# Performance work log

Hardware: AMD Instinct MI355X
Metric: run time of the kernel (lower is better)

Reference implementation:

```python
import jax, jax.numpy as jnp
import numpy as np

N_NODES = 50000
N_EDGES = 800000
D_FEAT = 128
DIM_H = 128
N_LAYERS = 3
N_CLASSES = 10
N_GRAPHS = 512


def setup_inputs() -> dict:
    key = jax.random.key(0)
    ks = jax.random.split(key, 8)
    x = jax.random.normal(ks[0], (N_NODES, D_FEAT), dtype=jnp.float32)
    W = jax.random.normal(ks[1], (N_LAYERS, DIM_H, DIM_H), dtype=jnp.float32) * 0.1
    b = jnp.zeros((N_LAYERS, DIM_H), dtype=jnp.float32)
    lin_w = jax.random.normal(ks[2], (DIM_H, N_CLASSES), dtype=jnp.float32) * 0.1
    lin_b = jnp.zeros((N_CLASSES,), dtype=jnp.float32)
    edge_index = jax.random.randint(ks[3], (2, N_EDGES), 0, N_NODES, dtype=jnp.int64)
    batch = jnp.sort(jax.random.randint(ks[4], (N_NODES,), 0, N_GRAPHS, dtype=jnp.int64))
    return {"x": x, "W": W, "b": b, "lin_w": lin_w, "lin_b": lin_b,
            "edge_index": edge_index, "batch": batch, "num_layers": N_LAYERS}


def _gcn_norm(edge_index, n_nodes):
    # add self loops (PyG GCNConv default), then symmetric normalization
    loop = jnp.arange(n_nodes, dtype=edge_index.dtype)
    src = jnp.concatenate([edge_index[0], loop])  # [E+N]
    dst = jnp.concatenate([edge_index[1], loop])
    deg = jax.ops.segment_sum(jnp.ones_like(dst, dtype=jnp.float32), dst,
                              num_segments=n_nodes)
    dinv = jnp.where(deg > 0, jax.lax.rsqrt(deg), 0.0)
    norm = dinv[src] * dinv[dst]  # [E+N]
    return src, dst, norm


def _gcn_conv(h, Wi, bi, src, dst, norm, n_nodes):
    h = h @ Wi                       # [N, dim_h] dense GEMM
    msg = h[src] * norm[:, None]     # gather + scale, [E+N, dim_h]
    out = jax.ops.segment_sum(msg, dst, num_segments=n_nodes)  # scatter-add
    return out + bi


def reference(x, W, b, lin_w, lin_b, edge_index, batch, num_layers):
    n_nodes = x.shape[0]
    src, dst, norm = _gcn_norm(edge_index, n_nodes)
    h = x
    for i in range(num_layers):
        h = jax.nn.relu(_gcn_conv(h, W[i], b[i], src, dst, norm, n_nodes))
    # global mean pool over graph ids
    sums = jax.ops.segment_sum(h, batch, num_segments=N_GRAPHS)          # [G, dim_h]
    cnts = jax.ops.segment_sum(jnp.ones((n_nodes,), h.dtype), batch,
                               num_segments=N_GRAPHS)
    hG = sums / jnp.maximum(cnts, 1.0)[:, None]
    # dropout is identity at eval; num_layers > 1 branch applies the linear head
    logits = hG @ lin_w + lin_b
    return hG, jax.nn.log_softmax(logits, axis=1)
```

## Files before the change

### kernel.cpp

```cpp
#include <hip/hip_runtime.h>
#include <hip/hip_bf16.h>
#include <hip/hip_fp8.h>

#define NN 50000
#define NE 800000
#define FD 128
#define NG 512
#define NC 10
#define NL 3
#define CAP 64
#define WT_B 192
#define E1_B 3125
#define GEMM_B 782

typedef unsigned short u16;
typedef unsigned char u8;
typedef unsigned int u32;
typedef short bf16x8 __attribute__((ext_vector_type(8)));
typedef float f32x4 __attribute__((ext_vector_type(4)));

__device__ __forceinline__ float b2f(u16 v) {
    union { u32 u; float f; } c; c.u = ((u32)v) << 16; return c.f;
}
__device__ __forceinline__ u16 f2b(float f) {
    __hip_bfloat16 h = __float2bfloat16(f);
    return *(u16*)&h;
}
__device__ __forceinline__ float p2f(u8 b) {
    __hip_fp8_e4m3 h; h.__x = b; return (float)h;
}
__device__ __forceinline__ u8 f2p(float f) {
    __hip_fp8_e4m3 h(f); return h.__x;
}

__global__ __launch_bounds__(256) void k_fillcvt(const int* __restrict__ src,
                                                 const int* __restrict__ dst,
                                                 int* __restrict__ cnt,
                                                 int* __restrict__ bkt,
                                                 const float* __restrict__ W,
                                                 u16* __restrict__ wt) {
    const int bid = blockIdx.x;
    if (bid < E1_B) {
        const int e = bid * 256 + threadIdx.x;
        const int d = dst[e];
        const int slot = atomicAdd(&cnt[d], 1);
        if (slot < CAP) bkt[d * CAP + slot] = src[e];
    } else {
        const int i = (bid - E1_B) * 256 + threadIdx.x;
        const int l = i >> 14, r = i & 16383, k = r >> 7, n = r & 127;
        wt[(l << 14) + n * FD + k] = f2b(W[i]);
    }
}

__global__ __launch_bounds__(256) void k_gemm0(const float* __restrict__ x,
                                               const u16* __restrict__ WT,
                                               const int* __restrict__ cnt,
                                               float* __restrict__ dinv,
                                               u8* __restrict__ Bout) {
    const int wid = blockIdx.x * 4 + (threadIdx.x >> 6);
    if (wid >= 3125) return;
    const int row0 = wid * 16;
    const int lane = threadIdx.x & 63;
    const int m = lane & 15;
    const int q = lane >> 4;
    f32x4 acc[8];
#pragma unroll
    for (int ct = 0; ct < 8; ++ct) acc[ct] = (f32x4){0.f, 0.f, 0.f, 0.f};
    const float* arow = x + (size_t)(row0 + m) * FD + q * 8;
    const u16* wrow = WT + (size_t)m * FD + q * 8;
#pragma unroll
    for (int kb = 0; kb < 4; ++kb) {
        const float4 p0 = *(const float4*)(arow + kb * 32);
        const float4 p1 = *(const float4*)(arow + kb * 32 + 4);
        bf16x8 af;
        af[0] = (short)f2b(p0.x); af[1] = (short)f2b(p0.y);
        af[2] = (short)f2b(p0.z); af[3] = (short)f2b(p0.w);
        af[4] = (short)f2b(p1.x); af[5] = (short)f2b(p1.y);
        af[6] = (short)f2b(p1.z); af[7] = (short)f2b(p1.w);
#pragma unroll
        for (int ct = 0; ct < 8; ++ct) {
            bf16x8 bf = *(const bf16x8*)(wrow + (size_t)ct * 16 * FD + kb * 32);
            acc[ct] = __builtin_amdgcn_mfma_f32_16x16x32_bf16(af, bf, acc[ct], 0, 0, 0);
        }
    }
    float dsc[4];
#pragma unroll
    for (int r = 0; r < 4; ++r) {
        dsc[r] = rsqrtf((float)(cnt[row0 + q * 4 + r] + 1));
        if (m == 0) dinv[row0 + q * 4 + r] = dsc[r];
    }
#pragma unroll
    for (int ct = 0; ct < 8; ++ct)
#pragma unroll
        for (int r = 0; r < 4; ++r)
            Bout[(size_t)(row0 + q * 4 + r) * FD + ct * 16 + m] =
                f2p(acc[ct][r] * dsc[r]);
}

__device__ __forceinline__ float4 gather_node4(const int rs, const int re,
                                               const int* __restrict__ bkt,
                                               const u8* __restrict__ B,
                                               const float di, const int n,
                                               const float4 bb, const int f) {
    const uchar4 vs = *(const uchar4*)(B + (size_t)n * FD + f);
    float a0 = 0.f, a1 = 0.f, a2 = 0.f, a3 = 0.f;
    float b0 = 0.f, b1 = 0.f, b2 = 0.f, b3 = 0.f;
    float c0 = 0.f, c1 = 0.f, c2 = 0.f, c3 = 0.f;
    float d0 = 0.f, d1 = 0.f, d2 = 0.f, d3 = 0.f;
    int e = rs;
    for (; e + 4 <= re; e += 4) {
        const int s0 = bkt[e];
        const int s1 = bkt[e + 1];
        const int s2 = bkt[e + 2];
        const int s3 = bkt[e + 3];
        const uchar4 v0 = *(const uchar4*)(B + (size_t)s0 * FD + f);
        const uchar4 v1 = *(const uchar4*)(B + (size_t)s1 * FD + f);
        const uchar4 v2 = *(const uchar4*)(B + (size_t)s2 * FD + f);
        const uchar4 v3 = *(const uchar4*)(B + (size_t)s3 * FD + f);
        a0 += p2f(v0.x); a1 += p2f(v0.y); a2 += p2f(v0.z); a3 += p2f(v0.w);
        b0 += p2f(v1.x); b1 += p2f(v1.y); b2 += p2f(v1.z); b3 += p2f(v1.w);
        c0 += p2f(v2.x); c1 += p2f(v2.y); c2 += p2f(v2.z); c3 += p2f(v2.w);
        d0 += p2f(v3.x); d1 += p2f(v3.y); d2 += p2f(v3.z); d3 += p2f(v3.w);
    }
    for (; e < re; ++e) {
        const int s0 = bkt[e];
        const uchar4 v0 = *(const uchar4*)(B + (size_t)s0 * FD + f);
        a0 += p2f(v0.x); a1 += p2f(v0.y); a2 += p2f(v0.z); a3 += p2f(v0.w);
    }
    a0 += b0 + c0 + d0 + p2f(vs.x);
    a1 += b1 + c1 + d1 + p2f(vs.y);
    a2 += b2 + c2 + d2 + p2f(vs.z);
    a3 += b3 + c3 + d3 + p2f(vs.w);
    float4 r;
    r.x = fmaxf(a0 * di + bb.x, 0.f);
    r.y = fmaxf(a1 * di + bb.y, 0.f);
    r.z = fmaxf(a2 * di + bb.z, 0.f);
    r.w = fmaxf(a3 * di + bb.w, 0.f);
    return r;
}

__global__ __launch_bounds__(512) void k_gg(const int* __restrict__ cnt,
                                            const int* __restrict__ bkt,
                                            const u8* __restrict__ Bin,
                                            const float* __restrict__ dinv,
                                            const float* __restrict__ bias,
                                            const u16* __restrict__ WTn,
                                            u8* __restrict__ Bout) {
    __shared__ u16 sA[16][FD + 8];
    const int tid = threadIdx.x;
    const int wave = tid >> 6;
    const int lane = tid & 63;
    const int nb = blockIdx.x * 16;
    {
        const int half = lane >> 5;
        const int n = nb + wave * 2 + half;
        const int f = (lane & 31) * 4;
        const int rs = n * CAP;
        const int re = rs + cnt[n];
        const float di = dinv[n];
        const float4 bb = *(const float4*)(bias + f);
        const float4 r = gather_node4(rs, re, bkt, Bin, di, n, bb, f);
        ushort4 o;
        o.x = f2b(r.x); o.y = f2b(r.y); o.z = f2b(r.z); o.w = f2b(r.w);
        *(ushort4*)&sA[wave * 2 + half][f] = o;
    }
    __syncthreads();
    const int ct = wave;
    const int m = lane & 15;
    const int q = lane >> 4;
    f32x4 acc = (f32x4){0.f, 0.f, 0.f, 0.f};
    const u16* wrow = WTn + (size_t)m * FD + q * 8 + (size_t)ct * 16 * FD;
#pragma unroll
    for (int kb = 0; kb < 4; ++kb) {
        bf16x8 af = *(const bf16x8*)&sA[m][q * 8 + kb * 32];
        bf16x8 bf = *(const bf16x8*)(wrow + kb * 32);
        acc = __builtin_amdgcn_mfma_f32_16x16x32_bf16(af, bf, acc, 0, 0, 0);
    }
    float dsc[4];
#pragma unroll
    for (int r = 0; r < 4; ++r) dsc[r] = dinv[nb + q * 4 + r];
#pragma unroll
    for (int r = 0; r < 4; ++r)
        Bout[(size_t)(nb + q * 4 + r) * FD + ct * 16 + m] =
            f2p(acc[r] * dsc[r]);
}

__global__ __launch_bounds__(1024) void k_gpool(const int* __restrict__ cnt,
                                                const int* __restrict__ bkt,
                                                const u8* __restrict__ B,
                                                const float* __restrict__ dinv,
                                                const float* __restrict__ bias,
                                                const int* __restrict__ batch,
                                                const float* __restrict__ lin_w,
                                                const float* __restrict__ lin_b,
                                                float* __restrict__ out) {
    __shared__ float sfeat[32][FD + 4];
    __shared__ float hm[FD];
    __shared__ int bnd[2];
    __shared__ float part2[2 * NC];
    const int g = blockIdx.x;
    const int tid = threadIdx.x;
    const int lane = tid & 63;
    const int slot = (tid >> 6) * 2 + (lane >> 5);
    const int f = (lane & 31) * 4;
    if (tid < 2) {
        const int key = g + tid;
        int lo = 0, hi = NN;
        while (lo < hi) {
            const int mid = (lo + hi) >> 1;
            if (batch[mid] < key) lo = mid + 1; else hi = mid;
        }
        bnd[tid] = lo;
    }
    __syncthreads();
    const int r0 = bnd[0], r1 = bnd[1];
    const float4 bb = *(const float4*)(bias + f);
    float s0 = 0.f, s1 = 0.f, s2 = 0.f, s3 = 0.f;
    for (int r = r0 + slot; r < r1; r += 32) {
        const int rs = r * CAP;
        const float4 v = gather_node4(rs, rs + cnt[r], bkt, B,
                                      dinv[r], r, bb, f);
        s0 += v.x; s1 += v.y; s2 += v.z; s3 += v.w;
    }
    sfeat[slot][f] = s0;
    sfeat[slot][f + 1] = s1;
    sfeat[slot][f + 2] = s2;
    sfeat[slot][f + 3] = s3;
    __syncthreads();
    if (tid < 128) {
        float tot = 0.f;
#pragma unroll
        for (int s = 0; s < 32; ++s) tot += sfeat[s][tid];
        const float mean = tot / fmaxf((float)(r1 - r0), 1.0f);
        hm[tid] = mean;
        out[(size_t)g * FD + tid] = mean;
    }
    __syncthreads();
    if (tid < 128) {
        const float hv = hm[tid];
        const int wv = tid >> 6;
#pragma unroll
        for (int c = 0; c < NC; ++c) {
            float p = hv * lin_w[tid * NC + c];
#pragma unroll
            for (int o = 32; o > 0; o >>= 1) p += __shfl_down(p, o, 64);
            if ((tid & 63) == 0) part2[c * 2 + wv] = p;
        }
    }
    __syncthreads();
    if (tid == 0) {
        float lg[NC];
        float m = -1e30f;
#pragma unroll
        for (int c = 0; c < NC; ++c) {
            lg[c] = part2[2 * c] + part2[2 * c + 1] + lin_b[c];
            m = fmaxf(m, lg[c]);
        }
        float s = 0.f;
#pragma unroll
        for (int c = 0; c < NC; ++c) s += expf(lg[c] - m);
        const float lse = m + logf(s);
        float* o = out + (size_t)NG * FD + (size_t)g * NC;
#pragma unroll
        for (int c = 0; c < NC; ++c) o[c] = lg[c] - lse;
    }
}

extern "C" void kernel_launch(void* const* d_in, const int* in_sizes, int n_in,
                              void* d_out, int out_size, void* d_ws, size_t ws_size,
                              hipStream_t stream) {
    const float* x     = (const float*)d_in[0];
    const float* W     = (const float*)d_in[1];
    const float* bias  = (const float*)d_in[2];
    const float* lin_w = (const float*)d_in[3];
    const float* lin_b = (const float*)d_in[4];
    const int*   src   = (const int*)d_in[5];
    const int*   dst   = src + NE;
    const int*   batch = (const int*)d_in[6];

    u8*    B0     = (u8*)d_ws;
    u8*    B1     = B0 + (size_t)NN * FD;
    u16*   WT     = (u16*)(B1 + (size_t)NN * FD);
    int*   bkt    = (int*)(WT + (size_t)NL * FD * FD);
    int*   cnt    = bkt + (size_t)NN * CAP;
    float* dinv   = (float*)(cnt + NN);
    float* out    = (float*)d_out;

    hipMemsetAsync(cnt, 0, NN * sizeof(int), stream);
    k_fillcvt<<<E1_B + WT_B, 256, 0, stream>>>(src, dst, cnt, bkt, W, WT);
    k_gemm0<<<GEMM_B, 256, 0, stream>>>(x, WT, cnt, dinv, B0);

    k_gg<<<NN / 16, 512, 0, stream>>>(cnt, bkt, B0, dinv, bias,
                                      WT + (size_t)1 * FD * FD, B1);
    k_gg<<<NN / 16, 512, 0, stream>>>(cnt, bkt, B1, dinv, bias + FD,
                                      WT + (size_t)2 * FD * FD, B0);
    k_gpool<<<NG, 1024, 0, stream>>>(cnt, bkt, B0, dinv, bias + 2 * FD,
                                     batch, lin_w, lin_b, out);
}
```

Before: 257.3 us.

## Fuse edge bucketing and first GEMM into one kernel, apply source normalization at gather

Merges the edge-bucket fill, weight transpose, and layer-0 GEMM into a single interleaved launch. The layer-0 GEMM now reads fp32 W directly with strided loads and no longer needs degree counts. Because of that, the source-side degree scaling moves out of the GEMM epilogue and into the gather, where each neighbor's rsqrt(cnt+1) is recomputed per edge. This drops one kernel launch and the dinv array, and lets bucket atomics overlap the GEMM. In exchange it adds an extra random cnt load per edge and keeps fp8 storage of the values before normalization, which changes their scaling.

New measurement: 263.9 us. 1.03x slower.

```diff
diff --git a/kernel.cpp b/kernel.cpp
--- a/kernel.cpp
+++ b/kernel.cpp
@@ -9,9 +9,10 @@
 #define NC 10
 #define NL 3
 #define CAP 64
-#define WT_B 192
 #define E1_B 3125
 #define GEMM_B 782
+#define CVT_B 128
+#define FRONT_B 4550
 
 typedef unsigned short u16;
 typedef unsigned char u8;
@@ -33,72 +34,72 @@
     __hip_fp8_e4m3 h(f); return h.__x;
 }
 
-__global__ __launch_bounds__(256) void k_fillcvt(const int* __restrict__ src,
-                                                 const int* __restrict__ dst,
-                                                 int* __restrict__ cnt,
-                                                 int* __restrict__ bkt,
-                                                 const float* __restrict__ W,
-                                                 u16* __restrict__ wt) {
+__global__ __launch_bounds__(256) void k_front(const int* __restrict__ src,
+                                               const int* __restrict__ dst,
+                                               int* __restrict__ cnt,
+                                               int* __restrict__ bkt,
+                                               const float* __restrict__ W,
+                                               u16* __restrict__ wt,
+                                               const float* __restrict__ x,
+                                               u8* __restrict__ Bout) {
     const int bid = blockIdx.x;
-    if (bid < E1_B) {
-        const int e = bid * 256 + threadIdx.x;
+    const int r5 = bid % 5;
+    const int q5 = bid / 5;
+    if (r5 != 0) {
+        const int sid = q5 * 4 + (r5 - 1);
+        if (sid >= E1_B) return;
+        const int e = sid * 256 + threadIdx.x;
         const int d = dst[e];
         const int slot = atomicAdd(&cnt[d], 1);
         if (slot < CAP) bkt[d * CAP + slot] = src[e];
+    } else if (q5 < GEMM_B) {
+        const int wid = q5 * 4 + (threadIdx.x >> 6);
+        if (wid >= 3125) return;
+        const int row0 = wid * 16;
+        const int lane = threadIdx.x & 63;
+        const int m = lane & 15;
+        const int q = lane >> 4;
+        f32x4 acc[8];
+#pragma unroll
+        for (int ct = 0; ct < 8; ++ct) acc[ct] = (f32x4){0.f, 0.f, 0.f, 0.f};
+        const float* arow = x + (size_t)(row0 + m) * FD + q * 8;
+        const float* wbase = W + (size_t)q * 8 * FD + m;
+#pragma unroll
+        for (int kb = 0; kb < 4; ++kb) {
+            const float4 p0 = *(const float4*)(arow + kb * 32);
+            const float4 p1 = *(const float4*)(arow + kb * 32 + 4);
+            bf16x8 af;
+            af[0] = (short)f2b(p0.x); af[1] = (short)f2b(p0.y);
+            af[2] = (short)f2b(p0.z); af[3] = (short)f2b(p0.w);
+            af[4] = (short)f2b(p1.x); af[5] = (short)f2b(p1.y);
+            af[6] = (short)f2b(p1.z); af[7] = (short)f2b(p1.w);
+#pragma unroll
+            for (int ct = 0; ct < 8; ++ct) {
+                const float* wp = wbase + (size_t)kb * 32 * FD + ct * 16;
+                bf16x8 bf;
+#pragma unroll
+                for (int j = 0; j < 8; ++j)
+                    bf[j] = (short)f2b(wp[(size_t)j * FD]);
+                acc[ct] = __builtin_amdgcn_mfma_f32_16x16x32_bf16(af, bf,
+                                                                  acc[ct], 0, 0, 0);
+            }
+        }
+#pragma unroll
+        for (int ct = 0; ct < 8; ++ct)
+#pragma unroll
+            for (int r = 0; r < 4; ++r)
+                Bout[(size_t)(row0 + q * 4 + r) * FD + ct * 16 + m] =
+                    f2p(acc[ct][r]);
     } else {
-        const int i = (bid - E1_B) * 256 + threadIdx.x;
-        const int l = i >> 14, r = i & 16383, k = r >> 7, n = r & 127;
-        wt[(l << 14) + n * FD + k] = f2b(W[i]);
-    }
-}
-
-__global__ __launch_bounds__(256) void k_gemm0(const float* __restrict__ x,
-                                               const u16* __restrict__ WT,
-                                               const int* __restrict__ cnt,
-                                               float* __restrict__ dinv,
-                                               u8* __restrict__ Bout) {
-    const int wid = blockIdx.x * 4 + (threadIdx.x >> 6);
-    if (wid >= 3125) return;
-    const int row0 = wid * 16;
-    const int lane = threadIdx.x & 63;
-    const int m = lane & 15;
-    const int q = lane >> 4;
-    f32x4 acc[8];
-#pragma unroll
-    for (int ct = 0; ct < 8; ++ct) acc[ct] = (f32x4){0.f, 0.f, 0.f, 0.f};
-    const float* arow = x + (size_t)(row0 + m) * FD + q * 8;
-    const u16* wrow = WT + (size_t)m * FD + q * 8;
-#pragma unroll
-    for (int kb = 0; kb < 4; ++kb) {
-        const float4 p0 = *(const float4*)(arow + kb * 32);
-        const float4 p1 = *(const float4*)(arow + kb * 32 + 4);
-        bf16x8 af;
-        af[0] = (short)f2b(p0.x); af[1] = (short)f2b(p0.y);
-        af[2] = (short)f2b(p0.z); af[3] = (short)f2b(p0.w);
-        af[4] = (short)f2b(p1.x); af[5] = (short)f2b(p1.y);
-        af[6] = (short)f2b(p1.z); af[7] = (short)f2b(p1.w);
-#pragma unroll
-        for (int ct = 0; ct < 8; ++ct) {
-            bf16x8 bf = *(const bf16x8*)(wrow + (size_t)ct * 16 * FD + kb * 32);
-            acc[ct] = __builtin_amdgcn_mfma_f32_16x16x32_bf16(af, bf, acc[ct], 0, 0, 0);
-        }
-    }
-    float dsc[4];
-#pragma unroll
-    for (int r = 0; r < 4; ++r) {
-        dsc[r] = rsqrtf((float)(cnt[row0 + q * 4 + r] + 1));
-        if (m == 0) dinv[row0 + q * 4 + r] = dsc[r];
-    }
-#pragma unroll
-    for (int ct = 0; ct < 8; ++ct)
-#pragma unroll
-        for (int r = 0; r < 4; ++r)
-            Bout[(size_t)(row0 + q * 4 + r) * FD + ct * 16 + m] =
-                f2p(acc[ct][r] * dsc[r]);
+        const int c = (q5 - GEMM_B) * 256 + threadIdx.x + FD * FD;
+        const int l = c >> 14, rr = c & 16383, k = rr >> 7, n = rr & 127;
+        wt[(l << 14) + n * FD + k] = f2b(W[c]);
+    }
 }
 
 __device__ __forceinline__ float4 gather_node4(const int rs, const int re,
                                                const int* __restrict__ bkt,
+                                               const int* __restrict__ cnt,
                                                const u8* __restrict__ B,
                                                const float di, const int n,
                                                const float4 bb, const int f) {
@@ -113,36 +114,45 @@
         const int s1 = bkt[e + 1];
         const int s2 = bkt[e + 2];
         const int s3 = bkt[e + 3];
+        const float w0 = rsqrtf((float)(cnt[s0] + 1));
+        const float w1 = rsqrtf((float)(cnt[s1] + 1));
+        const float w2 = rsqrtf((float)(cnt[s2] + 1));
+        const float w3 = rsqrtf((float)(cnt[s3] + 1));
         const uchar4 v0 = *(const uchar4*)(B + (size_t)s0 * FD + f);
         const uchar4 v1 = *(const uchar4*)(B + (size_t)s1 * FD + f);
         const uchar4 v2 = *(const uchar4*)(B + (size_t)s2 * FD + f);
         const uchar4 v3 = *(const uchar4*)(B + (size_t)s3 * FD + f);
-        a0 += p2f(v0.x); a1 += p2f(v0.y); a2 += p2f(v0.z); a3 += p2f(v0.w);
-        b0 += p2f(v1.x); b1 += p2f(v1.y); b2 += p2f(v1.z); b3 += p2f(v1.w);
-        c0 += p2f(v2.x); c1 += p2f(v2.y); c2 += p2f(v2.z); c3 += p2f(v2.w);
-        d0 += p2f(v3.x); d1 += p2f(v3.y); d2 += p2f(v3.z); d3 += p2f(v3.w);
+        a0 = fmaf(w0, p2f(v0.x), a0); a1 = fmaf(w0, p2f(v0.y), a1);
+        a2 = fmaf(w0, p2f(v0.z), a2); a3 = fmaf(w0, p2f(v0.w), a3);
+        b0 = fmaf(w1, p2f(v1.x), b0); b1 = fmaf(w1, p2f(v1.y), b1);
+        b2 = fmaf(w1, p2f(v1.z), b2); b3 = fmaf(w1, p2f(v1.w), b3);
+        c0 = fmaf(w2, p2f(v2.x), c0); c1 = fmaf(w2, p2f(v2.y), c1);
+        c2 = fmaf(w2, p2f(v2.z), c2); c3 = fmaf(w2, p2f(v2.w), c3);
+        d0 = fmaf(w3, p2f(v3.x), d0); d1 = fmaf(w3, p2f(v3.y), d1);
+        d2 = fmaf(w3, p2f(v3.z), d2); d3 = fmaf(w3, p2f(v3.w), d3);
     }
     for (; e < re; ++e) {
         const int s0 = bkt[e];
+        const float w0 = rsqrtf((float)(cnt[s0] + 1));
         const uchar4 v0 = *(const uchar4*)(B + (size_t)s0 * FD + f);
-        a0 += p2f(v0.x); a1 += p2f(v0.y); a2 += p2f(v0.z); a3 += p2f(v0.w);
-    }
-    a0 += b0 + c0 + d0 + p2f(vs.x);
-    a1 += b1 + c1 + d1 + p2f(vs.y);
-    a2 += b2 + c2 + d2 + p2f(vs.z);
-    a3 += b3 + c3 + d3 + p2f(vs.w);
+        a0 = fmaf(w0, p2f(v0.x), a0); a1 = fmaf(w0, p2f(v0.y), a1);
+        a2 = fmaf(w0, p2f(v0.z), a2); a3 = fmaf(w0, p2f(v0.w), a3);
+    }
+    a0 += b0 + c0 + d0 + di * p2f(vs.x);
+    a1 += b1 + c1 + d1 + di * p2f(vs.y);
+    a2 += b2 + c2 + d2 + di * p2f(vs.z);
+    a3 += b3 + c3 + d3 + di * p2f(vs.w);
     float4 r;
-    r.x = fmaxf(a0 * di + bb.x, 0.f);
-    r.y = fmaxf(a1 * di + bb.y, 0.f);
-    r.z = fmaxf(a2 * di + bb.z, 0.f);
-    r.w = fmaxf(a3 * di + bb.w, 0.f);
+    r.x = fmaxf(fmaf(a0, di, bb.x), 0.f);
+    r.y = fmaxf(fmaf(a1, di, bb.y), 0.f);
+    r.z = fmaxf(fmaf(a2, di, bb.z), 0.f);
+    r.w = fmaxf(fmaf(a3, di, bb.w), 0.f);
     return r;
 }
 
 __global__ __launch_bounds__(512) void k_gg(const int* __restrict__ cnt,
                                             const int* __restrict__ bkt,
                                             const u8* __restrict__ Bin,
-                                            const float* __restrict__ dinv,
                                             const float* __restrict__ bias,
                                             const u16* __restrict__ WTn,
                                             u8* __restrict__ Bout) {
@@ -155,11 +165,11 @@
         const int half = lane >> 5;
         const int n = nb + wave * 2 + half;
         const int f = (lane & 31) * 4;
+        const int cn = cnt[n];
         const int rs = n * CAP;
-        const int re = rs + cnt[n];
-        const float di = dinv[n];
+        const float di = rsqrtf((float)(cn + 1));
         const float4 bb = *(const float4*)(bias + f);
-        const float4 r = gather_node4(rs, re, bkt, Bin, di, n, bb, f);
+        const float4 r = gather_node4(rs, rs + cn, bkt, cnt, Bin, di, n, bb, f);
         ushort4 o;
         o.x = f2b(r.x); o.y = f2b(r.y); o.z = f2b(r.z); o.w = f2b(r.w);
         *(ushort4*)&sA[wave * 2 + half][f] = o;
@@ -176,19 +186,14 @@
         bf16x8 bf = *(const bf16x8*)(wrow + kb * 32);
         acc = __builtin_amdgcn_mfma_f32_16x16x32_bf16(af, bf, acc, 0, 0, 0);
     }
-    float dsc[4];
-#pragma unroll
-    for (int r = 0; r < 4; ++r) dsc[r] = dinv[nb + q * 4 + r];
 #pragma unroll
     for (int r = 0; r < 4; ++r)
-        Bout[(size_t)(nb + q * 4 + r) * FD + ct * 16 + m] =
-            f2p(acc[r] * dsc[r]);
+        Bout[(size_t)(nb + q * 4 + r) * FD + ct * 16 + m] = f2p(acc[r]);
 }
 
 __global__ __launch_bounds__(1024) void k_gpool(const int* __restrict__ cnt,
                                                 const int* __restrict__ bkt,
                                                 const u8* __restrict__ B,
-                                                const float* __restrict__ dinv,
                                                 const float* __restrict__ bias,
                                                 const int* __restrict__ batch,
                                                 const float* __restrict__ lin_w,
@@ -217,9 +222,10 @@
     const float4 bb = *(const float4*)(bias + f);
     float s0 = 0.f, s1 = 0.f, s2 = 0.f, s3 = 0.f;
     for (int r = r0 + slot; r < r1; r += 32) {
+        const int cn = cnt[r];
         const int rs = r * CAP;
-        const float4 v = gather_node4(rs, rs + cnt[r], bkt, B,
-                                      dinv[r], r, bb, f);
+        const float di = rsqrtf((float)(cn + 1));
+        const float4 v = gather_node4(rs, rs + cn, bkt, cnt, B, di, r, bb, f);
         s0 += v.x; s1 += v.y; s2 += v.z; s3 += v.w;
     }
     sfeat[slot][f] = s0;
@@ -283,17 +289,15 @@
     u16*   WT     = (u16*)(B1 + (size_t)NN * FD);
     int*   bkt    = (int*)(WT + (size_t)NL * FD * FD);
     int*   cnt    = bkt + (size_t)NN * CAP;
-    float* dinv   = (float*)(cnt + NN);
     float* out    = (float*)d_out;
 
     hipMemsetAsync(cnt, 0, NN * sizeof(int), stream);
-    k_fillcvt<<<E1_B + WT_B, 256, 0, stream>>>(src, dst, cnt, bkt, W, WT);
-    k_gemm0<<<GEMM_B, 256, 0, stream>>>(x, WT, cnt, dinv, B0);
-
-    k_gg<<<NN / 16, 512, 0, stream>>>(cnt, bkt, B0, dinv, bias,
+    k_front<<<FRONT_B, 256, 0, stream>>>(src, dst, cnt, bkt, W, WT, x, B0);
+
+    k_gg<<<NN / 16, 512, 0, stream>>>(cnt, bkt, B0, bias,
                                       WT + (size_t)1 * FD * FD, B1);
-    k_gg<<<NN / 16, 512, 0, stream>>>(cnt, bkt, B1, dinv, bias + FD,
+    k_gg<<<NN / 16, 512, 0, stream>>>(cnt, bkt, B1, bias + FD,
                                       WT + (size_t)2 * FD * FD, B0);
-    k_gpool<<<NG, 1024, 0, stream>>>(cnt, bkt, B0, dinv, bias + 2 * FD,
+    k_gpool<<<NG, 1024, 0, stream>>>(cnt, bkt, B0, bias + 2 * FD,
                                      batch, lin_w, lin_b, out);
 }
```
